# Kernel tuning notes

Hardware: AMD Instinct MI355X
Metric: run time of the kernel (lower is better)

## Reference

```python
import math
import jax, jax.numpy as jnp
import numpy as np

B, T, C = 2, 2048, 1024
HEADS = 16
HD = C // HEADS  # 64


def setup_inputs() -> dict:
    key = jax.random.key(0)
    ks = jax.random.split(key, 5)
    s = 0.02
    return {
        "x": jax.random.normal(ks[0], (B, T, C), jnp.float32),
        "Wq": jax.random.normal(ks[1], (C, C), jnp.float32) * s,
        "bq": jnp.zeros((C,), jnp.float32),
        "Wk": jax.random.normal(ks[2], (C, HD), jnp.float32) * s,
        "bk": jnp.zeros((HD,), jnp.float32),
        "Wv": jax.random.normal(ks[3], (C, HD), jnp.float32) * s,
        "bv": jnp.zeros((HD,), jnp.float32),
        "Wo": jax.random.normal(ks[4], (C, C), jnp.float32) * s,
        "bo": jnp.zeros((C,), jnp.float32),
    }


def _rope_tables(seq_len, dim):
    pos = jnp.arange(seq_len, dtype=jnp.float32)
    freqs = 1.0 / (10000.0 ** (jnp.arange(0, dim, 2, dtype=jnp.float32) / dim))
    ang = pos[:, None] * freqs[None, :]          # (T, dim//2)
    # broadcast over (B, T, H, dim//2)
    return jnp.sin(ang)[None, :, None, :], jnp.cos(ang)[None, :, None, :]


def _apply_rope(t, sin, cos, dim):
    t1, t2 = t[..., : dim // 2], t[..., dim // 2 :]
    # matches torch source: emb[..., :d/2]=sin, emb[..., d/2:]=cos
    return jnp.concatenate([t1 * cos + t2 * sin, t1 * sin - t2 * cos], axis=-1)


def reference(x, Wq, bq, Wk, bk, Wv, bv, Wo, bo):
    Bx, Tx, Cx = x.shape
    q = (x @ Wq + bq).reshape(Bx, Tx, HEADS, HD)   # (B,T,H,hd)
    k = (x @ Wk + bk)[:, :, None, :]               # (B,T,1,hd) single KV head (MQA)
    v = (x @ Wv + bv)[:, :, None, :]
    sin, cos = _rope_tables(Tx, HD)
    q = _apply_rope(q, sin, cos, HD)
    k = _apply_rope(k, sin, cos, HD)
    att = jnp.einsum('bthd,bThd->bhtT', q, k) / math.sqrt(HD)
    causal = jnp.triu(jnp.ones((Tx, Tx), bool), 1)
    att = jnp.where(causal, -jnp.inf, att)
    att = jax.nn.softmax(att, axis=-1)
    out = jnp.einsum('bhtT,bThd->bthd', att, v).reshape(Bx, Tx, Cx)
    return out @ Wo + bo
```

## Files before the change

### kernel.cpp

```cpp
#include <hip/hip_runtime.h>
#include <math.h>

#define BSZ   2
#define TSEQ  2048
#define CDIM  1024
#define NHEAD 16
#define HDIM  64
#define BT    (BSZ*TSEQ)
#define NQKV  1152

typedef __attribute__((ext_vector_type(8))) short short8;
typedef __attribute__((ext_vector_type(4))) float f32x4;
typedef unsigned short u16;
typedef unsigned int   u32;

__device__ __forceinline__ u16 f2b(float f) {
    union { float f; u32 u; } c; c.f = f;
    u32 u = c.u;
    u += 0x7fffu + ((u >> 16) & 1u);
    return (u16)(u >> 16);
}
__device__ __forceinline__ u32 pack2(float lo, float hi) {
    return (u32)f2b(lo) | ((u32)f2b(hi) << 16);
}

__device__ __forceinline__ void async_copy16(const void* g, void* l) {
    __builtin_amdgcn_global_load_lds(
        (__attribute__((address_space(1))) const void*)g,
        (__attribute__((address_space(3))) void*)l,
        16, 0, 0);
}

__global__ __launch_bounds__(256) void cast_bf16_kernel(
    const float* __restrict__ src, u16* __restrict__ dst, int n4)
{
    int i = blockIdx.x * 256 + threadIdx.x;
    if (i >= n4) return;
    float4 f = ((const float4*)src)[i];
    u16* d = dst + (size_t)i * 4;
    d[0] = f2b(f.x); d[1] = f2b(f.y); d[2] = f2b(f.z); d[3] = f2b(f.w);
}

__device__ __forceinline__ void transpose_tile(
    const float* __restrict__ W, u16* __restrict__ Wt,
    int K, int Nw, int nofs, int bx, int by, float (*T)[65])
{
    const int tid = threadIdx.x;
    const int k0 = by * 64, n0 = bx * 64;
    #pragma unroll
    for (int i = 0; i < 16; ++i) {
        int idx = i * 256 + tid, r = idx >> 6, c = idx & 63;
        T[r][c] = W[(size_t)(k0 + r) * Nw + n0 + c];
    }
    __syncthreads();
    #pragma unroll
    for (int i = 0; i < 16; ++i) {
        int idx = i * 256 + tid, rn = idx >> 6, ck = idx & 63;
        Wt[(size_t)(nofs + n0 + rn) * K + k0 + ck] = f2b(T[ck][rn]);
    }
}

__global__ __launch_bounds__(256) void prep_kernel(
    const float* __restrict__ Wq, const float* __restrict__ Wk,
    const float* __restrict__ Wv, const float* __restrict__ Wo,
    const float* __restrict__ bq, const float* __restrict__ bk,
    const float* __restrict__ bv,
    u16* __restrict__ Wqkvt, u16* __restrict__ Wot, float* __restrict__ bqkv)
{
    __shared__ float T[64][65];
    const int bid = blockIdx.x;
    if (bid < 256) {
        transpose_tile(Wq, Wqkvt, 1024, 1024, 0, bid & 15, bid >> 4, T);
    } else if (bid < 272) {
        transpose_tile(Wk, Wqkvt, 1024, 64, 1024, 0, bid - 256, T);
    } else if (bid < 288) {
        transpose_tile(Wv, Wqkvt, 1024, 64, 1088, 0, bid - 272, T);
    } else if (bid < 544) {
        int b2 = bid - 288;
        transpose_tile(Wo, Wot, 1024, 1024, 0, b2 & 15, b2 >> 4, T);
    } else {
        for (int i = threadIdx.x; i < NQKV; i += 256)
            bqkv[i] = (i < 1024) ? bq[i] : (i < 1088 ? bk[i - 1024] : bv[i - 1088]);
    }
}

__global__ __launch_bounds__(256) void gemm_qkv_kernel(
    const u16* __restrict__ A, const u16* __restrict__ Bt,
    const float* __restrict__ bias,
    u16* __restrict__ qb, u16* __restrict__ kb, u16* __restrict__ vT)
{
    __shared__ __align__(16) u16 AsC[64 * 32];
    __shared__ __align__(16) u16 BsC[128 * 32];
    const int tid  = threadIdx.x;
    const int wave = tid >> 6, lane = tid & 63;
    const int ln16 = lane & 15, quad = lane >> 4;
    const int wm = wave >> 1, wn = wave & 1;
    const int m0 = blockIdx.y * 64, n0 = blockIdx.x * 128;
    const int K = CDIM;

    const int c_row = ((tid >> 6) << 4) + (tid & 15);
    const int c_k   = ((tid >> 4) & 3) * 8;
    const u16* ag  = &A [(size_t)(m0 + c_row)       * K + c_k];
    const u16* bg0 = &Bt[(size_t)(n0 + c_row)       * K + c_k];
    const u16* bg1 = &Bt[(size_t)(n0 + 64 + c_row)  * K + c_k];
    u16* a_l  = &AsC[(size_t)wave * 64 * 8];
    u16* b_l0 = &BsC[(size_t)wave * 64 * 8];
    u16* b_l1 = &BsC[(size_t)(wave + 4) * 64 * 8];

    f32x4 acc[2][4];
    #pragma unroll
    for (int i = 0; i < 2; ++i)
        #pragma unroll
        for (int j = 0; j < 4; ++j) acc[i][j] = (f32x4){0.f, 0.f, 0.f, 0.f};

    for (int k0 = 0; k0 < K; k0 += 32) {
        async_copy16(ag,  a_l);
        async_copy16(bg0, b_l0);
        async_copy16(bg1, b_l1);
        ag += 32; bg0 += 32; bg1 += 32;
        __syncthreads();

        short8 af[2], bf[4];
        #pragma unroll
        for (int mt = 0; mt < 2; ++mt)
            af[mt] = *(const short8*)&AsC[(((wm * 2 + mt) * 64) + quad * 16 + ln16) * 8];
        #pragma unroll
        for (int nt = 0; nt < 4; ++nt)
            bf[nt] = *(const short8*)&BsC[(((wn * 4 + nt) * 64) + quad * 16 + ln16) * 8];
        #pragma unroll
        for (int mt = 0; mt < 2; ++mt)
            #pragma unroll
            for (int nt = 0; nt < 4; ++nt)
                acc[mt][nt] = __builtin_amdgcn_mfma_f32_16x16x32_bf16(
                    af[mt], bf[nt], acc[mt][nt], 0, 0, 0);
        __syncthreads();
    }

    #pragma unroll
    for (int mt = 0; mt < 2; ++mt)
        #pragma unroll
        for (int nt = 0; nt < 4; ++nt) {
            float bb = bias[n0 + wn * 64 + nt * 16 + ln16];
            #pragma unroll
            for (int r = 0; r < 4; ++r) acc[mt][nt][r] += bb;
        }

    const int col0 = n0 + wn * 64;
    if (col0 < 1024) {
        const int hh = col0 >> 6;
        #pragma unroll
        for (int nt = 0; nt < 2; ++nt) {
            int j = nt * 16 + ln16;
            float fr = exp2f(-0.41524101186092029f * (float)j);
            #pragma unroll
            for (int mt = 0; mt < 2; ++mt)
                #pragma unroll
                for (int r = 0; r < 4; ++r) {
                    int m = m0 + wm * 32 + mt * 16 + quad * 4 + r;
                    float sn, cs;
                    __sincosf((float)(m & (TSEQ - 1)) * fr, &sn, &cs);
                    float t1 = acc[mt][nt][r], t2 = acc[mt][nt + 2][r];
                    u16* o = qb + (size_t)m * CDIM + hh * 64 + j;
                    o[0]  = f2b(fmaf(t1, cs,  t2 * sn) * 0.18033688011112043f);
                    o[32] = f2b(fmaf(t1, sn, -t2 * cs) * 0.18033688011112043f);
                }
        }
    } else if (wn == 0) {
        #pragma unroll
        for (int nt = 0; nt < 2; ++nt) {
            int j = nt * 16 + ln16;
            float fr = exp2f(-0.41524101186092029f * (float)j);
            #pragma unroll
            for (int mt = 0; mt < 2; ++mt)
                #pragma unroll
                for (int r = 0; r < 4; ++r) {
                    int m = m0 + wm * 32 + mt * 16 + quad * 4 + r;
                    float sn, cs;
                    __sincosf((float)(m & (TSEQ - 1)) * fr, &sn, &cs);
                    float t1 = acc[mt][nt][r], t2 = acc[mt][nt + 2][r];
                    u16* o = kb + (size_t)m * HDIM + j;
                    o[0]  = f2b(fmaf(t1, cs,  t2 * sn));
                    o[32] = f2b(fmaf(t1, sn, -t2 * cs));
                }
        }
    } else {
        #pragma unroll
        for (int nt = 0; nt < 4; ++nt) {
            int d = nt * 16 + ln16;
            #pragma unroll
            for (int mt = 0; mt < 2; ++mt) {
                int mr = m0 + wm * 32 + mt * 16 + quad * 4;
                int b  = mr >> 11, tq = mr & (TSEQ - 1);
                uint2 val;
                val.x = pack2(acc[mt][nt][0], acc[mt][nt][1]);
                val.y = pack2(acc[mt][nt][2], acc[mt][nt][3]);
                *(uint2*)&vT[(size_t)(b * HDIM + d) * TSEQ + tq] = val;
            }
        }
    }
}

__global__ __launch_bounds__(256) void gemm_mfma_kernel(
    const u16* __restrict__ A, const u16* __restrict__ Bt,
    const float* __restrict__ bias, float* __restrict__ Y,
    int M, int N, int K)
{
    __shared__ __align__(16) u16 AsC[64 * 32];
    __shared__ __align__(16) u16 BsC[128 * 32];
    const int tid  = threadIdx.x;
    const int wave = tid >> 6, lane = tid & 63;
    const int ln16 = lane & 15, quad = lane >> 4;
    const int wm = wave >> 1, wn = wave & 1;
    const int m0 = blockIdx.y * 64, n0 = blockIdx.x * 128;

    const int c_row = ((tid >> 6) << 4) + (tid & 15);
    const int c_k   = ((tid >> 4) & 3) * 8;
    const u16* ag  = &A [(size_t)(m0 + c_row)       * K + c_k];
    const u16* bg0 = &Bt[(size_t)(n0 + c_row)       * K + c_k];
    const u16* bg1 = &Bt[(size_t)(n0 + 64 + c_row)  * K + c_k];
    u16* a_l  = &AsC[(size_t)wave * 64 * 8];
    u16* b_l0 = &BsC[(size_t)wave * 64 * 8];
    u16* b_l1 = &BsC[(size_t)(wave + 4) * 64 * 8];

    f32x4 acc[2][4];
    #pragma unroll
    for (int i = 0; i < 2; ++i)
        #pragma unroll
        for (int j = 0; j < 4; ++j) acc[i][j] = (f32x4){0.f, 0.f, 0.f, 0.f};

    for (int k0 = 0; k0 < K; k0 += 32) {
        async_copy16(ag,  a_l);
        async_copy16(bg0, b_l0);
        async_copy16(bg1, b_l1);
        ag += 32; bg0 += 32; bg1 += 32;
        __syncthreads();

        short8 af[2], bf[4];
        #pragma unroll
        for (int mt = 0; mt < 2; ++mt)
            af[mt] = *(const short8*)&AsC[(((wm * 2 + mt) * 64) + quad * 16 + ln16) * 8];
        #pragma unroll
        for (int nt = 0; nt < 4; ++nt)
            bf[nt] = *(const short8*)&BsC[(((wn * 4 + nt) * 64) + quad * 16 + ln16) * 8];
        #pragma unroll
        for (int mt = 0; mt < 2; ++mt)
            #pragma unroll
            for (int nt = 0; nt < 4; ++nt)
                acc[mt][nt] = __builtin_amdgcn_mfma_f32_16x16x32_bf16(
                    af[mt], bf[nt], acc[mt][nt], 0, 0, 0);
        __syncthreads();
    }

    #pragma unroll
    for (int mt = 0; mt < 2; ++mt)
        #pragma unroll
        for (int nt = 0; nt < 4; ++nt) {
            int n = n0 + wn * 64 + nt * 16 + ln16;
            float bb = bias[n];
            #pragma unroll
            for (int r = 0; r < 4; ++r) {
                int m = m0 + wm * 32 + mt * 16 + quad * 4 + r;
                Y[(size_t)m * N + n] = acc[mt][nt][r] + bb;
            }
        }
}

__device__ __forceinline__ void flash_stage_kv(
    const u16* __restrict__ kb, const u16* __restrict__ vT,
    int b, int kt, u16* __restrict__ Ksb, u16* __restrict__ Vsb,
    const int* row_c, const int* off_c, int c0)
{
    const size_t kt0 = (size_t)(b * TSEQ + kt * 64);
    #pragma unroll
    for (int hf = 0; hf < 2; ++hf) {
        int cc = c0 + hf * 256;
        async_copy16(kb + (kt0 + row_c[hf]) * HDIM + off_c[hf], Ksb + cc * 8);
        async_copy16(vT + (size_t)(b * HDIM + row_c[hf]) * TSEQ + kt * 64 + off_c[hf],
                     Vsb + cc * 8);
    }
}

__device__ __forceinline__ void flash_tile(
    const u16* __restrict__ Ksb, const u16* __restrict__ Vsb,
    const u16* __restrict__ Qs, u16* __restrict__ Pw,
    int wave, int ln16, int quad, bool diag,
    float* lsum, f32x4* oacc)
{
    f32x4 sv[4];
    #pragma unroll
    for (int t = 0; t < 4; ++t) sv[t] = (f32x4){0.f, 0.f, 0.f, 0.f};
    #pragma unroll
    for (int kk2 = 0; kk2 < 2; ++kk2) {
        short8 af = *(const short8*)&Qs[(wave * 128 + kk2 * 64 + quad * 16 + ln16) * 8];
        #pragma unroll
        for (int t = 0; t < 4; ++t) {
            short8 bf = *(const short8*)&Ksb[(t * 128 + kk2 * 64 + quad * 16 + ln16) * 8];
            sv[t] = __builtin_amdgcn_mfma_f32_16x16x32_bf16(af, bf, sv[t], 0, 0, 0);
        }
    }

    if (diag) {
        #pragma unroll
        for (int t = 0; t < 4; ++t) {
            int key = t * 16 + ln16;
            #pragma unroll
            for (int r = 0; r < 4; ++r) {
                float e = (key > wave * 16 + quad * 4 + r) ? 0.f : exp2f(sv[t][r]);
                lsum[r] += e;
                Pw[(quad * 4 + r) * 72 + t * 16 + ln16] = f2b(e);
            }
        }
    } else {
        #pragma unroll
        for (int t = 0; t < 4; ++t)
            #pragma unroll
            for (int r = 0; r < 4; ++r) {
                float e = exp2f(sv[t][r]);
                lsum[r] += e;
                Pw[(quad * 4 + r) * 72 + t * 16 + ln16] = f2b(e);
            }
    }

    #pragma unroll
    for (int kk2 = 0; kk2 < 2; ++kk2) {
        short8 pf = *(const short8*)&Pw[ln16 * 72 + kk2 * 32 + quad * 8];
        #pragma unroll
        for (int t = 0; t < 4; ++t) {
            short8 vf = *(const short8*)&Vsb[(t * 128 + kk2 * 64 + quad * 16 + ln16) * 8];
            oacc[t] = __builtin_amdgcn_mfma_f32_16x16x32_bf16(pf, vf, oacc[t], 0, 0, 0);
        }
    }
}

__global__ __launch_bounds__(256) void flash_mfma_kernel(
    const u16* __restrict__ qb, const u16* __restrict__ kb,
    const u16* __restrict__ vT, u16* __restrict__ o)
{
    const int id  = blockIdx.x;
    const int qt  = 31 - (id >> 5);
    const int hb  = id & 31;
    const int h   = hb >> 1;
    const int b   = hb & 1;
    __shared__ __align__(16) u16 Qs [512 * 8];
    __shared__ __align__(16) u16 Ks0[512 * 8];
    __shared__ __align__(16) u16 Ks1[512 * 8];
    __shared__ __align__(16) u16 Vs0[512 * 8];
    __shared__ __align__(16) u16 Vs1[512 * 8];
    __shared__ __align__(16) u16 Ps[4 * 16 * 72];

    const int tid  = threadIdx.x;
    const int wave = tid >> 6, lane = tid & 63;
    const int ln16 = lane & 15, quad = lane >> 4;

    const int c0 = tid;
    int row_c[2], off_c[2];
    #pragma unroll
    for (int hf = 0; hf < 2; ++hf) {
        int c = c0 + hf * 256;
        row_c[hf] = ((c >> 7) << 4) | (c & 15);
        off_c[hf] = ((c >> 6) & 1) * 32 + ((c >> 4) & 3) * 8;
    }

    u16* Pw = &Ps[wave * 16 * 72];

    #pragma unroll
    for (int hf = 0; hf < 2; ++hf)
        async_copy16(
            qb + (size_t)(b * TSEQ + qt * 64 + row_c[hf]) * CDIM + h * HDIM + off_c[hf],
            Qs + (c0 + hf * 256) * 8);
    flash_stage_kv(kb, vT, b, 0, Ks0, Vs0, row_c, off_c, c0);

    float lsum[4];
    f32x4 oacc[4];
    #pragma unroll
    for (int r = 0; r < 4; ++r) lsum[r] = 0.f;
    #pragma unroll
    for (int t = 0; t < 4; ++t) oacc[t] = (f32x4){0.f, 0.f, 0.f, 0.f};

    int kt = 0;
    while (true) {
        __syncthreads();
        if (kt < qt) flash_stage_kv(kb, vT, b, kt + 1, Ks1, Vs1, row_c, off_c, c0);
        flash_tile(Ks0, Vs0, Qs, Pw, wave, ln16, quad, kt == qt, lsum, oacc);
        if (++kt > qt) break;
        __syncthreads();
        if (kt < qt) flash_stage_kv(kb, vT, b, kt + 1, Ks0, Vs0, row_c, off_c, c0);
        flash_tile(Ks1, Vs1, Qs, Pw, wave, ln16, quad, kt == qt, lsum, oacc);
        if (++kt > qt) break;
    }

    float inv[4];
    #pragma unroll
    for (int r = 0; r < 4; ++r) {
        float l = lsum[r];
        #pragma unroll
        for (int off = 1; off < 16; off <<= 1)
            l += __shfl_xor(l, off, 64);
        inv[r] = 1.0f / l;
    }
    #pragma unroll
    for (int t = 0; t < 4; ++t) {
        #pragma unroll
        for (int r = 0; r < 4; ++r) {
            int row = qt * 64 + wave * 16 + quad * 4 + r;
            int d   = t * 16 + ln16;
            o[(size_t)(b * TSEQ + row) * CDIM + h * HDIM + d] = f2b(oacc[t][r] * inv[r]);
        }
    }
}

extern "C" void kernel_launch(void* const* d_in, const int* in_sizes, int n_in,
                              void* d_out, int out_size, void* d_ws, size_t ws_size,
                              hipStream_t stream)
{
    const float* x  = (const float*)d_in[0];
    const float* Wq = (const float*)d_in[1];
    const float* bq = (const float*)d_in[2];
    const float* Wk = (const float*)d_in[3];
    const float* bk = (const float*)d_in[4];
    const float* Wv = (const float*)d_in[5];
    const float* bv = (const float*)d_in[6];
    const float* Wo = (const float*)d_in[7];
    const float* bo = (const float*)d_in[8];
    float* out = (float*)d_out;

    const size_t MB = 1u << 20;
    char* w = (char*)d_ws;
    u16*   xb   = (u16*)(w);
    u16*   aob  = (u16*)(w);
    u16*   qb   = (u16*)(w + 8 * MB);
    u16*   kb   = (u16*)(w + 16 * MB);
    u16*   vT   = (u16*)(w + 16 * MB + 512 * 1024);
    u16*   Wqkvt= (u16*)(w + 17 * MB);
    u16*   Wot  = (u16*)(w + 20 * MB);
    float* bqkv = (float*)(w + 22 * MB);

    cast_bf16_kernel<<<dim3(BT * CDIM / 4 / 256), dim3(256), 0, stream>>>(
        x, xb, BT * CDIM / 4);
    prep_kernel<<<dim3(545), dim3(256), 0, stream>>>(Wq, Wk, Wv, Wo, bq, bk, bv,
                                                     Wqkvt, Wot, bqkv);
    gemm_qkv_kernel<<<dim3(NQKV / 128, BT / 64), dim3(256), 0, stream>>>(
        xb, Wqkvt, bqkv, qb, kb, vT);
    flash_mfma_kernel<<<dim3(32 * NHEAD * BSZ), dim3(256), 0, stream>>>(
        qb, kb, vT, aob);
    gemm_mfma_kernel<<<dim3(CDIM / 128, BT / 64), dim3(256), 0, stream>>>(
        aob, Wot, bo, out, BT, CDIM, CDIM);
}
```

Measured before the change: 192.7 us.

## Double-buffer GEMM shared tiles and hoist Q fragments into registers

Both MFMA GEMM kernels now use two shared-memory buffers for A and B. The next K-slice is loaded asynchronously while MFMAs run on the current one, which drops one barrier per iteration and hides global-load latency. The flash attention kernel loads its Q fragments into registers once before the KV loop instead of re-reading them from LDS on every tile. The costs are double the GEMM LDS footprint, which may reduce occupancy, and a few more live registers in attention.

```diff
diff --git a/kernel.cpp b/kernel.cpp
--- a/kernel.cpp
+++ b/kernel.cpp
@@ -84,13 +84,32 @@
     }
 }
 
+__device__ __forceinline__ void gemm_step(
+    const u16* __restrict__ AsC, const u16* __restrict__ BsC,
+    int wm, int wn, int quad, int ln16, f32x4 (*acc)[4])
+{
+    short8 af[2], bf[4];
+    #pragma unroll
+    for (int mt = 0; mt < 2; ++mt)
+        af[mt] = *(const short8*)&AsC[(((wm * 2 + mt) * 64) + quad * 16 + ln16) * 8];
+    #pragma unroll
+    for (int nt = 0; nt < 4; ++nt)
+        bf[nt] = *(const short8*)&BsC[(((wn * 4 + nt) * 64) + quad * 16 + ln16) * 8];
+    #pragma unroll
+    for (int mt = 0; mt < 2; ++mt)
+        #pragma unroll
+        for (int nt = 0; nt < 4; ++nt)
+            acc[mt][nt] = __builtin_amdgcn_mfma_f32_16x16x32_bf16(
+                af[mt], bf[nt], acc[mt][nt], 0, 0, 0);
+}
+
 __global__ __launch_bounds__(256) void gemm_qkv_kernel(
     const u16* __restrict__ A, const u16* __restrict__ Bt,
     const float* __restrict__ bias,
     u16* __restrict__ qb, u16* __restrict__ kb, u16* __restrict__ vT)
 {
-    __shared__ __align__(16) u16 AsC[64 * 32];
-    __shared__ __align__(16) u16 BsC[128 * 32];
+    __shared__ __align__(16) u16 As0[64 * 32],  As1[64 * 32];
+    __shared__ __align__(16) u16 Bs0[128 * 32], Bs1[128 * 32];
     const int tid  = threadIdx.x;
     const int wave = tid >> 6, lane = tid & 63;
     const int ln16 = lane & 15, quad = lane >> 4;
@@ -103,9 +122,7 @@
     const u16* ag  = &A [(size_t)(m0 + c_row)       * K + c_k];
     const u16* bg0 = &Bt[(size_t)(n0 + c_row)       * K + c_k];
     const u16* bg1 = &Bt[(size_t)(n0 + 64 + c_row)  * K + c_k];
-    u16* a_l  = &AsC[(size_t)wave * 64 * 8];
-    u16* b_l0 = &BsC[(size_t)wave * 64 * 8];
-    u16* b_l1 = &BsC[(size_t)(wave + 4) * 64 * 8];
+    const int ao = wave * 64 * 8, bo0 = wave * 64 * 8, bo1 = (wave + 4) * 64 * 8;
 
     f32x4 acc[2][4];
     #pragma unroll
@@ -113,27 +130,27 @@
         #pragma unroll
         for (int j = 0; j < 4; ++j) acc[i][j] = (f32x4){0.f, 0.f, 0.f, 0.f};
 
-    for (int k0 = 0; k0 < K; k0 += 32) {
-        async_copy16(ag,  a_l);
-        async_copy16(bg0, b_l0);
-        async_copy16(bg1, b_l1);
-        ag += 32; bg0 += 32; bg1 += 32;
-        __syncthreads();
-
-        short8 af[2], bf[4];
-        #pragma unroll
-        for (int mt = 0; mt < 2; ++mt)
-            af[mt] = *(const short8*)&AsC[(((wm * 2 + mt) * 64) + quad * 16 + ln16) * 8];
-        #pragma unroll
-        for (int nt = 0; nt < 4; ++nt)
-            bf[nt] = *(const short8*)&BsC[(((wn * 4 + nt) * 64) + quad * 16 + ln16) * 8];
-        #pragma unroll
-        for (int mt = 0; mt < 2; ++mt)
-            #pragma unroll
-            for (int nt = 0; nt < 4; ++nt)
-                acc[mt][nt] = __builtin_amdgcn_mfma_f32_16x16x32_bf16(
-                    af[mt], bf[nt], acc[mt][nt], 0, 0, 0);
-        __syncthreads();
+    async_copy16(ag, As0 + ao); async_copy16(bg0, Bs0 + bo0); async_copy16(bg1, Bs0 + bo1);
+    ag += 32; bg0 += 32; bg1 += 32;
+
+    int k0 = 0;
+    for (;;) {
+        __syncthreads();
+        if (k0 + 32 < K) {
+            async_copy16(ag, As1 + ao); async_copy16(bg0, Bs1 + bo0); async_copy16(bg1, Bs1 + bo1);
+            ag += 32; bg0 += 32; bg1 += 32;
+        }
+        gemm_step(As0, Bs0, wm, wn, quad, ln16, acc);
+        k0 += 32;
+        if (k0 >= K) break;
+        __syncthreads();
+        if (k0 + 32 < K) {
+            async_copy16(ag, As0 + ao); async_copy16(bg0, Bs0 + bo0); async_copy16(bg1, Bs0 + bo1);
+            ag += 32; bg0 += 32; bg1 += 32;
+        }
+        gemm_step(As1, Bs1, wm, wn, quad, ln16, acc);
+        k0 += 32;
+        if (k0 >= K) break;
     }
 
     #pragma unroll
@@ -205,8 +222,8 @@
     const float* __restrict__ bias, float* __restrict__ Y,
     int M, int N, int K)
 {
-    __shared__ __align__(16) u16 AsC[64 * 32];
-    __shared__ __align__(16) u16 BsC[128 * 32];
+    __shared__ __align__(16) u16 As0[64 * 32],  As1[64 * 32];
+    __shared__ __align__(16) u16 Bs0[128 * 32], Bs1[128 * 32];
     const int tid  = threadIdx.x;
     const int wave = tid >> 6, lane = tid & 63;
     const int ln16 = lane & 15, quad = lane >> 4;
@@ -218,9 +235,7 @@
     const u16* ag  = &A [(size_t)(m0 + c_row)       * K + c_k];
     const u16* bg0 = &Bt[(size_t)(n0 + c_row)       * K + c_k];
     const u16* bg1 = &Bt[(size_t)(n0 + 64 + c_row)  * K + c_k];
-    u16* a_l  = &AsC[(size_t)wave * 64 * 8];
-    u16* b_l0 = &BsC[(size_t)wave * 64 * 8];
-    u16* b_l1 = &BsC[(size_t)(wave + 4) * 64 * 8];
+    const int ao = wave * 64 * 8, bo0 = wave * 64 * 8, bo1 = (wave + 4) * 64 * 8;
 
     f32x4 acc[2][4];
     #pragma unroll
@@ -228,27 +243,27 @@
         #pragma unroll
         for (int j = 0; j < 4; ++j) acc[i][j] = (f32x4){0.f, 0.f, 0.f, 0.f};
 
-    for (int k0 = 0; k0 < K; k0 += 32) {
-        async_copy16(ag,  a_l);
-        async_copy16(bg0, b_l0);
-        async_copy16(bg1, b_l1);
-        ag += 32; bg0 += 32; bg1 += 32;
-        __syncthreads();
-
-        short8 af[2], bf[4];
-        #pragma unroll
-        for (int mt = 0; mt < 2; ++mt)
-            af[mt] = *(const short8*)&AsC[(((wm * 2 + mt) * 64) + quad * 16 + ln16) * 8];
-        #pragma unroll
-        for (int nt = 0; nt < 4; ++nt)
-            bf[nt] = *(const short8*)&BsC[(((wn * 4 + nt) * 64) + quad * 16 + ln16) * 8];
-        #pragma unroll
-        for (int mt = 0; mt < 2; ++mt)
-            #pragma unroll
-            for (int nt = 0; nt < 4; ++nt)
-                acc[mt][nt] = __builtin_amdgcn_mfma_f32_16x16x32_bf16(
-                    af[mt], bf[nt], acc[mt][nt], 0, 0, 0);
-        __syncthreads();
+    async_copy16(ag, As0 + ao); async_copy16(bg0, Bs0 + bo0); async_copy16(bg1, Bs0 + bo1);
+    ag += 32; bg0 += 32; bg1 += 32;
+
+    int k0 = 0;
+    for (;;) {
+        __syncthreads();
+        if (k0 + 32 < K) {
+            async_copy16(ag, As1 + ao); async_copy16(bg0, Bs1 + bo0); async_copy16(bg1, Bs1 + bo1);
+            ag += 32; bg0 += 32; bg1 += 32;
+        }
+        gemm_step(As0, Bs0, wm, wn, quad, ln16, acc);
+        k0 += 32;
+        if (k0 >= K) break;
+        __syncthreads();
+        if (k0 + 32 < K) {
+            async_copy16(ag, As0 + ao); async_copy16(bg0, Bs0 + bo0); async_copy16(bg1, Bs0 + bo1);
+            ag += 32; bg0 += 32; bg1 += 32;
+        }
+        gemm_step(As1, Bs1, wm, wn, quad, ln16, acc);
+        k0 += 32;
+        if (k0 >= K) break;
     }
 
     #pragma unroll
@@ -282,7 +297,7 @@
 
 __device__ __forceinline__ void flash_tile(
     const u16* __restrict__ Ksb, const u16* __restrict__ Vsb,
-    const u16* __restrict__ Qs, u16* __restrict__ Pw,
+    const short8* __restrict__ qf, u16* __restrict__ Pw,
     int wave, int ln16, int quad, bool diag,
     float* lsum, f32x4* oacc)
 {
@@ -291,11 +306,10 @@
     for (int t = 0; t < 4; ++t) sv[t] = (f32x4){0.f, 0.f, 0.f, 0.f};
     #pragma unroll
     for (int kk2 = 0; kk2 < 2; ++kk2) {
-        short8 af = *(const short8*)&Qs[(wave * 128 + kk2 * 64 + quad * 16 + ln16) * 8];
         #pragma unroll
         for (int t = 0; t < 4; ++t) {
             short8 bf = *(const short8*)&Ksb[(t * 128 + kk2 * 64 + quad * 16 + ln16) * 8];
-            sv[t] = __builtin_amdgcn_mfma_f32_16x16x32_bf16(af, bf, sv[t], 0, 0, 0);
+            sv[t] = __builtin_amdgcn_mfma_f32_16x16x32_bf16(qf[kk2], bf, sv[t], 0, 0, 0);
         }
     }
 
@@ -377,16 +391,21 @@
     #pragma unroll
     for (int t = 0; t < 4; ++t) oacc[t] = (f32x4){0.f, 0.f, 0.f, 0.f};
 
+    __syncthreads();
+    short8 qf[2];
+    qf[0] = *(const short8*)&Qs[(wave * 128 +  0 + quad * 16 + ln16) * 8];
+    qf[1] = *(const short8*)&Qs[(wave * 128 + 64 + quad * 16 + ln16) * 8];
+
     int kt = 0;
-    while (true) {
-        __syncthreads();
+    for (;;) {
         if (kt < qt) flash_stage_kv(kb, vT, b, kt + 1, Ks1, Vs1, row_c, off_c, c0);
-        flash_tile(Ks0, Vs0, Qs, Pw, wave, ln16, quad, kt == qt, lsum, oacc);
+        flash_tile(Ks0, Vs0, qf, Pw, wave, ln16, quad, kt == qt, lsum, oacc);
         if (++kt > qt) break;
         __syncthreads();
         if (kt < qt) flash_stage_kv(kb, vT, b, kt + 1, Ks0, Vs0, row_c, off_c, c0);
-        flash_tile(Ks1, Vs1, Qs, Pw, wave, ln16, quad, kt == qt, lsum, oacc);
+        flash_tile(Ks1, Vs1, qf, Pw, wave, ln16, quad, kt == qt, lsum, oacc);
         if (++kt > qt) break;
+        __syncthreads();
     }
 
     float inv[4];
```

Measured after the change: 198.1 us. 1.03x slower.
